# Optimization experiments

Hardware: AMD Instinct MI355X
Metric: run time of the kernel (lower is better)

The kernel has to match this reference:

```python
import jax, jax.numpy as jnp
import numpy as np

B, S, E, H, W = 4, 2048, 1024, 16, 128
HD = E // H

def setup_inputs() -> dict:
    key = jax.random.key(0)
    ks = jax.random.split(key, 5)
    scale = 1.0 / np.sqrt(E)
    x = jax.random.normal(ks[0], (B, S, E), dtype=jnp.float32)
    w_in = jax.random.uniform(ks[1], (3 * E, E), dtype=jnp.float32, minval=-scale, maxval=scale)
    b_in = jnp.zeros((3 * E,), dtype=jnp.float32)
    w_out = jax.random.uniform(ks[2], (E, E), dtype=jnp.float32, minval=-scale, maxval=scale)
    b_out = jnp.zeros((E,), dtype=jnp.float32)
    return {"x": x, "w_in": w_in, "b_in": b_in, "w_out": w_out, "b_out": b_out}

def reference(x, w_in, b_in, w_out, b_out):
    b, s, e = x.shape
    # fused QKV projection (torch MultiheadAttention in_proj)
    qkv = x @ w_in.T + b_in                      # [B,S,3E]
    q, k, v = jnp.split(qkv, 3, axis=-1)
    q = q.reshape(b, s, H, HD).transpose(0, 2, 1, 3)  # [B,H,S,HD]
    k = k.reshape(b, s, H, HD).transpose(0, 2, 1, 3)
    v = v.reshape(b, s, H, HD).transpose(0, 2, 1, 3)
    scores = jnp.einsum('bhqd,bhkd->bhqk', q, k) / jnp.sqrt(jnp.asarray(HD, x.dtype))
    # banded causal mask: row i attends to columns [i-W, i]
    i = jnp.arange(s)[:, None]
    j = jnp.arange(s)[None, :]
    allowed = (j <= i) & (j >= i - W)            # [S,S]
    scores = jnp.where(allowed[None, None], scores, jnp.asarray(-1e9, x.dtype))
    attn = jax.nn.softmax(scores, axis=-1)
    out = jnp.einsum('bhqk,bhkd->bhqd', attn, v)  # [B,H,S,HD]
    out = out.transpose(0, 2, 1, 3).reshape(b, s, e)
    return out @ w_out.T + b_out
```

## Files before the change

### kernel.cpp

```cpp
#include <hip/hip_runtime.h>
#include <stdint.h>

#define SLEN 2048
#define EMB  1024
#define NHEAD 16
#define HDIM  64
#define WINSZ 128

typedef __attribute__((ext_vector_type(8))) __bf16 bf16x8;
typedef __attribute__((ext_vector_type(4))) float  f32x4;

__device__ __forceinline__ unsigned short f2bf(float f) {
  union { float f; unsigned int u; } v;
  v.f = f;
  unsigned int r = v.u + 0x7FFFu + ((v.u >> 16) & 1u);
  return (unsigned short)(r >> 16);
}

__device__ __forceinline__ unsigned int pack_bf(float a, float b) {
  union { float f; unsigned int u; } x, y;
  x.f = a; y.f = b;
  return ((y.u + 0x8000u) & 0xFFFF0000u) | ((x.u + 0x8000u) >> 16);
}

__global__ void cvt_all(const float* __restrict__ x,
                        const float* __restrict__ wi,
                        const float* __restrict__ wo,
                        unsigned short* __restrict__ dst) {
  const long n0 = 8388608, n1 = n0 + 3145728, n2 = n1 + 1048576;
  const long stride = (long)gridDim.x * 256 * 4;
  for (long i = ((long)blockIdx.x * 256 + threadIdx.x) * 4; i < n2; i += stride) {
    const float* src; long off;
    if (i < n0)      { src = x;  off = i; }
    else if (i < n1) { src = wi; off = i - n0; }
    else             { src = wo; off = i - n1; }
    float4 f = *(const float4*)(src + off);
    ushort4 o;
    o.x = f2bf(f.x); o.y = f2bf(f.y); o.z = f2bf(f.z); o.w = f2bf(f.w);
    *(ushort4*)(dst + i) = o;
  }
}

#define AS1(p) (const __attribute__((address_space(1))) unsigned int*)((const void*)(p))
#define AS3(p) (__attribute__((address_space(3))) unsigned int*)((void*)(p))

template <int MODE>
__global__ __launch_bounds__(512, 2) void gemm_nt(
    const unsigned short* __restrict__ A,
    const unsigned short* __restrict__ B,
    const float* __restrict__ bias,
    void* __restrict__ Cout,
    unsigned short* __restrict__ vt,
    int M, int N, int K, int ldc)
{
  __shared__ unsigned short lds[73728];
  const int tid  = threadIdx.x;
  const int wave = tid >> 6, lane = tid & 63;
  const int quad = lane >> 4, l16 = lane & 15;
  const int wm = (wave >> 2) * 64, wn = (wave & 3) * 64;
  const int swz = l16 & 7;

  const int nwgx = gridDim.x;
  const int nwg  = nwgx * gridDim.y;
  const int orig = blockIdx.y * nwgx + blockIdx.x;
  const int bswz = (orig & 7) * (nwg >> 3) + (orig >> 3);
  const long mBase = (long)(bswz / nwgx) * 128;
  const long nBase = (long)(bswz % nwgx) * 256;

  const int lr  = lane >> 3;
  const int lks = ((lane & 7) ^ lr) * 8;
  const unsigned short* Abase = A + (mBase + lr) * (long)K + lks;
  const unsigned short* Bbase = B + (nBase + lr) * (long)K + lks;

#define STAGE3(TT, dstOff, H) do {                                                     \
    const long _kc = (long)(TT) * 64;                                                  \
    const int _ar = wave * 16 + (H) * 8;                                               \
    const int _br = wave * 32 + (H) * 16;                                              \
    __builtin_amdgcn_global_load_lds(AS1(Abase + (long)_ar * K + _kc),                 \
                                     AS3(lds + (dstOff) + _ar * 64), 16, 0, 0);        \
    __builtin_amdgcn_global_load_lds(AS1(Bbase + (long)_br * K + _kc),                 \
                                     AS3(lds + (dstOff) + 8192 + _br * 64), 16, 0, 0); \
    __builtin_amdgcn_global_load_lds(AS1(Bbase + (long)(_br + 8) * K + _kc),           \
                                     AS3(lds + (dstOff) + 8192 + (_br + 8) * 64), 16, 0, 0); \
  } while (0)

  f32x4 acc[4][4];
#pragma unroll
  for (int i = 0; i < 4; ++i)
#pragma unroll
    for (int j = 0; j < 4; ++j)
#pragma unroll
      for (int r = 0; r < 4; ++r) acc[i][j][r] = 0.f;

  const int NT = K >> 6;

  STAGE3(0, 0, 0); STAGE3(0, 0, 1);
  STAGE3(1, 24576, 0); STAGE3(1, 24576, 1);

  int curOff = 0, stgOff = 49152;
  for (int T = 0; T < NT; ++T) {
    if (T + 1 < NT) asm volatile("s_waitcnt vmcnt(6)" ::: "memory");
    else            asm volatile("s_waitcnt vmcnt(0)" ::: "memory");
    __builtin_amdgcn_s_barrier();
    __builtin_amdgcn_sched_barrier(0);

    const unsigned short* Ar = lds + curOff;
    const unsigned short* Br = lds + curOff + 8192;
    const bool doStage = (T + 2 < NT);

#pragma unroll
    for (int s = 0; s < 2; ++s) {
      bf16x8 aF[4], bF[4];
#pragma unroll
      for (int i = 0; i < 4; ++i)
        aF[i] = *(const bf16x8*)(Ar + (wm + i * 16 + l16) * 64 + (((s * 4 + quad) ^ swz) * 8));
#pragma unroll
      for (int j = 0; j < 4; ++j)
        bF[j] = *(const bf16x8*)(Br + (wn + j * 16 + l16) * 64 + (((s * 4 + quad) ^ swz) * 8));
      if (doStage) STAGE3(T + 2, stgOff, s);
      asm volatile("s_waitcnt lgkmcnt(0)" ::: "memory");
      __builtin_amdgcn_sched_barrier(0);
      __builtin_amdgcn_s_setprio(1);
#pragma unroll
      for (int i = 0; i < 4; ++i)
#pragma unroll
        for (int j = 0; j < 4; ++j)
          acc[i][j] = __builtin_amdgcn_mfma_f32_16x16x32_bf16(aF[i], bF[j], acc[i][j], 0, 0, 0);
      __builtin_amdgcn_s_setprio(0);
    }
    curOff = (curOff == 49152) ? 0 : curOff + 24576;
    stgOff = (stgOff == 49152) ? 0 : stgOff + 24576;
  }
#undef STAGE3

  if (MODE == 1 && nBase >= 2048) {
#pragma unroll
    for (int j = 0; j < 4; ++j) {
      const int nG = (int)nBase + wn + j * 16 + l16;
      const float bv = bias[nG];
      const int hd = nG - 2048;
      const int hh = hd >> 6, dd = hd & 63;
#pragma unroll
      for (int i = 0; i < 4; ++i) {
        const int mG0 = (int)mBase + wm + i * 16 + quad * 4;
        const int bb = mG0 >> 11, ss = mG0 & 2047;
        ushort4 o;
        o.x = f2bf(acc[i][j][0] + bv);
        o.y = f2bf(acc[i][j][1] + bv);
        o.z = f2bf(acc[i][j][2] + bv);
        o.w = f2bf(acc[i][j][3] + bv);
        *(ushort4*)(vt + (((long)(bb * NHEAD + hh)) * HDIM + dd) * SLEN + ss) = o;
      }
    }
  } else {
#pragma unroll
    for (int j = 0; j < 4; ++j) {
      const long nG = nBase + wn + j * 16 + l16;
      const float bv = bias[nG];
#pragma unroll
      for (int i = 0; i < 4; ++i)
#pragma unroll
        for (int r = 0; r < 4; ++r) {
          const long mG = mBase + wm + i * 16 + quad * 4 + r;
          const float v = acc[i][j][r] + bv;
          if (MODE == 1) ((unsigned short*)Cout)[mG * ldc + nG] = f2bf(v);
          else           ((float*)Cout)[mG * ldc + nG] = v;
        }
    }
  }
}

__global__ __launch_bounds__(512, 4) void local_attn(
    const unsigned short* __restrict__ qk,
    const unsigned short* __restrict__ vT,
    unsigned short* __restrict__ outw)
{
  const int qb = blockIdx.x;
  const int h  = blockIdx.y;
  const int b  = blockIdx.z;
  const int tid = threadIdx.x;
  const int wave = tid >> 6, lane = tid & 63;
  const int quad = lane >> 4, l16 = lane & 15;

  __shared__ unsigned short Klds[256 * 64];
  __shared__ unsigned short Vlds[64 * 256];

  const int kwin0 = qb * 128 - WINSZ;

  const int q0 = qb * 128 + wave * 16;
  const long qrow = (long)(b * SLEN + q0 + l16) * 2048 + h * HDIM;
  const bf16x8 qB0 = *(const bf16x8*)(qk + qrow + quad * 8);
  const bf16x8 qB1 = *(const bf16x8*)(qk + qrow + 32 + quad * 8);

  {
    const int kr = lane >> 3, kc = lane & 7;
    const long colOff = 1024 + h * HDIM + ((kc ^ kr) * 8);
#pragma unroll
    for (int t = 0; t < 4; ++t) {
      const int u = wave * 4 + t;
      const int sk = max(kwin0 + u * 8 + kr, 0);
      const unsigned short* g = qk + (long)(b * SLEN + sk) * 2048 + colOff;
      __builtin_amdgcn_global_load_lds(AS1(g), AS3(Klds + u * 512), 16, 0, 0);
    }
  }
  {
    const unsigned short* vbase = vT + ((long)(b * NHEAD + h)) * HDIM * SLEN;
#pragma unroll
    for (int t = 0; t < 4; ++t) {
      const int c = t * 512 + tid;
      const int d = c >> 5, k8 = c & 31;
      const int s0 = max(kwin0 + k8 * 8, 0);
      uint4 v = *(const uint4*)(vbase + (long)d * SLEN + s0);
      *(uint4*)(Vlds + d * 256 + ((k8 ^ (d & 7)) * 8)) = v;
    }
  }

  __syncthreads();

  const int lbase = (wave * 16) & ~31;
  const int kx = l16 & 7;
  const int a0 = (quad ^ kx) * 8;
  const int a1 = ((4 + quad) ^ kx) * 8;
  f32x4 sc[5][2];
#pragma unroll
  for (int it = 0; it < 5; ++it) {
    const int l0 = lbase + it * 32;
#pragma unroll
    for (int half = 0; half < 2; ++half) {
      const unsigned short* kr_ = Klds + (l0 + half * 16 + l16) * 64;
      const bf16x8 kA0 = *(const bf16x8*)(kr_ + a0);
      const bf16x8 kA1 = *(const bf16x8*)(kr_ + a1);
      f32x4 s;
#pragma unroll
      for (int r = 0; r < 4; ++r) s[r] = 0.f;
      __builtin_amdgcn_s_setprio(1);
      s = __builtin_amdgcn_mfma_f32_16x16x32_bf16(kA0, qB0, s, 0, 0, 0);
      s = __builtin_amdgcn_mfma_f32_16x16x32_bf16(kA1, qB1, s, 0, 0, 0);
      __builtin_amdgcn_s_setprio(0);
      sc[it][half] = s;
    }
  }

  const int qlocal = WINSZ + wave * 16 + l16;
  const int lo = max(wave * 16 + l16, kwin0 < 0 ? -kwin0 : 0);
  const int kb = lbase + quad * 4;
  float m = -3.0e38f;
#pragma unroll
  for (int it = 0; it < 5; ++it)
#pragma unroll
    for (int half = 0; half < 2; ++half)
#pragma unroll
      for (int r = 0; r < 4; ++r) {
        const int kl = kb + it * 32 + half * 16 + r;
        float v = sc[it][half][r] * 0.125f;
        v = (kl >= lo && kl <= qlocal) ? v : -3.0e38f;
        sc[it][half][r] = v;
        m = fmaxf(m, v);
      }
  m = fmaxf(m, __shfl_xor(m, 16, 64));
  m = fmaxf(m, __shfl_xor(m, 32, 64));

  float lsum = 0.f;
#pragma unroll
  for (int it = 0; it < 5; ++it)
#pragma unroll
    for (int half = 0; half < 2; ++half)
#pragma unroll
      for (int r = 0; r < 4; ++r) {
        const float e = __expf(sc[it][half][r] - m);
        sc[it][half][r] = e;
        lsum += e;
      }
  lsum += __shfl_xor(lsum, 16, 64);
  lsum += __shfl_xor(lsum, 32, 64);
  const float invl = 1.0f / lsum;

  f32x4 Oacc[4];
#pragma unroll
  for (int dt = 0; dt < 4; ++dt)
#pragma unroll
    for (int r = 0; r < 4; ++r) Oacc[dt][r] = 0.f;

#pragma unroll
  for (int it = 0; it < 5; ++it) {
    const int l0 = lbase + it * 32;
    const unsigned int u0 = pack_bf(sc[it][0][0], sc[it][0][1]);
    const unsigned int u1 = pack_bf(sc[it][0][2], sc[it][0][3]);
    const unsigned int u2 = pack_bf(sc[it][1][0], sc[it][1][1]);
    const unsigned int u3 = pack_bf(sc[it][1][2], sc[it][1][3]);
    unsigned int breg[4];
#pragma unroll
    for (int r = 0; r < 4; ++r) {
      const int srcl = ((quad & 1) * 2 + (r >> 1)) * 16 + l16;
      const unsigned int ga = __shfl((int)((r & 1) ? u1 : u0), srcl, 64);
      const unsigned int gb = __shfl((int)((r & 1) ? u3 : u2), srcl, 64);
      breg[r] = (quad >> 1) ? gb : ga;
    }
    union { unsigned int u[4]; bf16x8 v; } pB;
    pB.u[0] = breg[0]; pB.u[1] = breg[1]; pB.u[2] = breg[2]; pB.u[3] = breg[3];

    const int chBase = (l0 >> 3);
#pragma unroll
    for (int dt = 0; dt < 4; ++dt) {
      const int ch = (chBase + quad) ^ kx;
      const bf16x8 vA = *(const bf16x8*)(Vlds + (dt * 16 + l16) * 256 + ch * 8);
      __builtin_amdgcn_s_setprio(1);
      Oacc[dt] = __builtin_amdgcn_mfma_f32_16x16x32_bf16(vA, pB.v, Oacc[dt], 0, 0, 0);
      __builtin_amdgcn_s_setprio(0);
    }
  }

  const long obase = (long)(b * SLEN + q0 + l16) * EMB + h * HDIM;
#pragma unroll
  for (int dt = 0; dt < 4; ++dt) {
    ushort4 o;
    o.x = f2bf(Oacc[dt][0] * invl);
    o.y = f2bf(Oacc[dt][1] * invl);
    o.z = f2bf(Oacc[dt][2] * invl);
    o.w = f2bf(Oacc[dt][3] * invl);
    *(ushort4*)(outw + obase + dt * 16 + quad * 4) = o;
  }
}

extern "C" void kernel_launch(void* const* d_in, const int* in_sizes, int n_in,
                              void* d_out, int out_size, void* d_ws, size_t ws_size,
                              hipStream_t stream) {
  const float* x     = (const float*)d_in[0];
  const float* w_in  = (const float*)d_in[1];
  const float* b_in  = (const float*)d_in[2];
  const float* w_out = (const float*)d_in[3];
  const float* b_out = (const float*)d_in[4];
  float* out = (float*)d_out;

  char* ws = (char*)d_ws;
  unsigned short* xb    = (unsigned short*)(ws + 0);
  unsigned short* winb  = (unsigned short*)(ws + 16777216);
  unsigned short* woutb = (unsigned short*)(ws + 23068672);
  unsigned short* qkb   = (unsigned short*)(ws + 25165824);
  unsigned short* attn  = (unsigned short*)(ws + 58720256);
  unsigned short* vT    = (unsigned short*)(ws + 75497472);

  cvt_all<<<2048, 256, 0, stream>>>(x, w_in, w_out, xb);

  gemm_nt<1><<<dim3(3072 / 256, 8192 / 128), 512, 0, stream>>>(
      xb, winb, b_in, (void*)qkb, vT, 8192, 3072, 1024, 2048);

  local_attn<<<dim3(SLEN / 128, NHEAD, 4), 512, 0, stream>>>(qkb, vT, attn);

  gemm_nt<0><<<dim3(1024 / 256, 8192 / 128), 512, 0, stream>>>(
      attn, woutb, b_out, (void*)out, nullptr, 8192, 1024, 1024, 1024);
}
```

Measured before the change: 201.5 us.

## Fold softmax scale into Q projection, stage P in LDS, read V directly from global

The QKV GEMM epilogue now multiplies Q by scale*log2(e), so the attention kernel can drop its per-score multiply and use exp2f. The separate V LDS buffer is removed. V fragments are loaded straight from global memory into MFMA operands, and the probability matrix is written into the reused K LDS region instead of being rearranged with lane shuffles. This cuts LDS use and the shuffle work, which may allow more blocks per CU. In exchange it adds an extra barrier and uncoalesced, uncached global loads for V, and the s_setprio hints are dropped.

```diff
diff --git a/kernel.cpp b/kernel.cpp
--- a/kernel.cpp
+++ b/kernel.cpp
@@ -157,12 +157,13 @@
     for (int j = 0; j < 4; ++j) {
       const long nG = nBase + wn + j * 16 + l16;
       const float bv = bias[nG];
+      const float qs = (MODE == 1 && nG < 1024) ? 0.18033688011f : 1.0f;
 #pragma unroll
       for (int i = 0; i < 4; ++i)
 #pragma unroll
         for (int r = 0; r < 4; ++r) {
           const long mG = mBase + wm + i * 16 + quad * 4 + r;
-          const float v = acc[i][j][r] + bv;
+          const float v = (acc[i][j][r] + bv) * qs;
           if (MODE == 1) ((unsigned short*)Cout)[mG * ldc + nG] = f2bf(v);
           else           ((float*)Cout)[mG * ldc + nG] = v;
         }
@@ -182,8 +183,7 @@
   const int wave = tid >> 6, lane = tid & 63;
   const int quad = lane >> 4, l16 = lane & 15;
 
-  __shared__ unsigned short Klds[256 * 64];
-  __shared__ unsigned short Vlds[64 * 256];
+  __shared__ unsigned short KP[21504];
 
   const int kwin0 = qb * 128 - WINSZ;
 
@@ -200,18 +200,7 @@
       const int u = wave * 4 + t;
       const int sk = max(kwin0 + u * 8 + kr, 0);
       const unsigned short* g = qk + (long)(b * SLEN + sk) * 2048 + colOff;
-      __builtin_amdgcn_global_load_lds(AS1(g), AS3(Klds + u * 512), 16, 0, 0);
-    }
-  }
-  {
-    const unsigned short* vbase = vT + ((long)(b * NHEAD + h)) * HDIM * SLEN;
-#pragma unroll
-    for (int t = 0; t < 4; ++t) {
-      const int c = t * 512 + tid;
-      const int d = c >> 5, k8 = c & 31;
-      const int s0 = max(kwin0 + k8 * 8, 0);
-      uint4 v = *(const uint4*)(vbase + (long)d * SLEN + s0);
-      *(uint4*)(Vlds + d * 256 + ((k8 ^ (d & 7)) * 8)) = v;
+      __builtin_amdgcn_global_load_lds(AS1(g), AS3(KP + u * 512), 16, 0, 0);
     }
   }
 
@@ -227,19 +216,19 @@
     const int l0 = lbase + it * 32;
 #pragma unroll
     for (int half = 0; half < 2; ++half) {
-      const unsigned short* kr_ = Klds + (l0 + half * 16 + l16) * 64;
+      const unsigned short* kr_ = KP + (l0 + half * 16 + l16) * 64;
       const bf16x8 kA0 = *(const bf16x8*)(kr_ + a0);
       const bf16x8 kA1 = *(const bf16x8*)(kr_ + a1);
       f32x4 s;
 #pragma unroll
       for (int r = 0; r < 4; ++r) s[r] = 0.f;
-      __builtin_amdgcn_s_setprio(1);
       s = __builtin_amdgcn_mfma_f32_16x16x32_bf16(kA0, qB0, s, 0, 0, 0);
       s = __builtin_amdgcn_mfma_f32_16x16x32_bf16(kA1, qB1, s, 0, 0, 0);
-      __builtin_amdgcn_s_setprio(0);
       sc[it][half] = s;
     }
   }
+
+  __syncthreads();
 
   const int qlocal = WINSZ + wave * 16 + l16;
   const int lo = max(wave * 16 + l16, kwin0 < 0 ? -kwin0 : 0);
@@ -252,7 +241,7 @@
 #pragma unroll
       for (int r = 0; r < 4; ++r) {
         const int kl = kb + it * 32 + half * 16 + r;
-        float v = sc[it][half][r] * 0.125f;
+        float v = sc[it][half][r];
         v = (kl >= lo && kl <= qlocal) ? v : -3.0e38f;
         sc[it][half][r] = v;
         m = fmaxf(m, v);
@@ -267,7 +256,7 @@
     for (int half = 0; half < 2; ++half)
 #pragma unroll
       for (int r = 0; r < 4; ++r) {
-        const float e = __expf(sc[it][half][r] - m);
+        const float e = exp2f(sc[it][half][r] - m);
         sc[it][half][r] = e;
         lsum += e;
       }
@@ -275,6 +264,18 @@
   lsum += __shfl_xor(lsum, 32, 64);
   const float invl = 1.0f / lsum;
 
+  const int pbase = wave * 2688 + l16 * 168;
+#pragma unroll
+  for (int it = 0; it < 5; ++it)
+#pragma unroll
+    for (int half = 0; half < 2; ++half) {
+      uint2 w;
+      w.x = pack_bf(sc[it][half][0], sc[it][half][1]);
+      w.y = pack_bf(sc[it][half][2], sc[it][half][3]);
+      *(uint2*)(KP + pbase + it * 32 + half * 16 + quad * 4) = w;
+    }
+
+  const unsigned short* vbase = vT + ((long)(b * NHEAD + h)) * HDIM * SLEN;
   f32x4 Oacc[4];
 #pragma unroll
   for (int dt = 0; dt < 4; ++dt)
@@ -283,30 +284,12 @@
 
 #pragma unroll
   for (int it = 0; it < 5; ++it) {
-    const int l0 = lbase + it * 32;
-    const unsigned int u0 = pack_bf(sc[it][0][0], sc[it][0][1]);
-    const unsigned int u1 = pack_bf(sc[it][0][2], sc[it][0][3]);
-    const unsigned int u2 = pack_bf(sc[it][1][0], sc[it][1][1]);
-    const unsigned int u3 = pack_bf(sc[it][1][2], sc[it][1][3]);
-    unsigned int breg[4];
-#pragma unroll
-    for (int r = 0; r < 4; ++r) {
-      const int srcl = ((quad & 1) * 2 + (r >> 1)) * 16 + l16;
-      const unsigned int ga = __shfl((int)((r & 1) ? u1 : u0), srcl, 64);
-      const unsigned int gb = __shfl((int)((r & 1) ? u3 : u2), srcl, 64);
-      breg[r] = (quad >> 1) ? gb : ga;
-    }
-    union { unsigned int u[4]; bf16x8 v; } pB;
-    pB.u[0] = breg[0]; pB.u[1] = breg[1]; pB.u[2] = breg[2]; pB.u[3] = breg[3];
-
-    const int chBase = (l0 >> 3);
+    const bf16x8 pB = *(const bf16x8*)(KP + pbase + it * 32 + quad * 8);
+    const int sb = max(kwin0 + lbase + it * 32 + quad * 8, 0);
 #pragma unroll
     for (int dt = 0; dt < 4; ++dt) {
-      const int ch = (chBase + quad) ^ kx;
-      const bf16x8 vA = *(const bf16x8*)(Vlds + (dt * 16 + l16) * 256 + ch * 8);
-      __builtin_amdgcn_s_setprio(1);
-      Oacc[dt] = __builtin_amdgcn_mfma_f32_16x16x32_bf16(vA, pB.v, Oacc[dt], 0, 0, 0);
-      __builtin_amdgcn_s_setprio(0);
+      const bf16x8 vA = *(const bf16x8*)(vbase + (long)(dt * 16 + l16) * SLEN + sb);
+      Oacc[dt] = __builtin_amdgcn_mfma_f32_16x16x32_bf16(vA, pB, Oacc[dt], 0, 0, 0);
     }
   }
 
```

Measured after the change: 202.8 us. Within noise of the previous version (+0.6%).
